# Performance work log

Measured on AMD Instinct MI355X. Metric: run time of the kernel, lower is better.

Reference implementation:

```python
import jax, jax.numpy as jnp
import numpy as np

B, T, D, H = 2, 2048, 1024, 16
HD = D // H

def setup_inputs() -> dict:
    key = jax.random.key(0)
    ks = jax.random.split(key, 5)
    fan = D
    bound_w = float(np.sqrt(6.0 / fan))  # kaiming_uniform-ish scale
    return {
        "x": jax.random.normal(ks[0], (B, T, D), dtype=jnp.float32),
        "W_qkv": jax.random.uniform(ks[1], (3 * D, D), minval=-bound_w, maxval=bound_w, dtype=jnp.float32),
        "b_qkv": jax.random.uniform(ks[2], (3 * D,), minval=-bound_w, maxval=bound_w, dtype=jnp.float32),
        "W_proj": jax.random.uniform(ks[3], (D, D), minval=-bound_w, maxval=bound_w, dtype=jnp.float32),
        "b_proj": jax.random.uniform(ks[4], (D,), minval=-bound_w, maxval=bound_w, dtype=jnp.float32),
    }

def reference(x, W_qkv, b_qkv, W_proj, b_proj):
    Bx, Tx, C = x.shape
    h, hd = H, C // H
    qkv = x @ W_qkv.T + b_qkv                      # (B,T,3C)
    q, k, v = jnp.split(qkv, 3, axis=-1)
    # (B,T,C) -> (B,h,T,hd)
    q = q.reshape(Bx, Tx, h, hd).transpose(0, 2, 1, 3)
    k = k.reshape(Bx, Tx, h, hd).transpose(0, 2, 1, 3)
    v = v.reshape(Bx, Tx, h, hd).transpose(0, 2, 1, 3)
    scale = hd ** -0.5
    scores = jnp.einsum('bhqd,bhkd->bhqk', q, k) * scale
    causal = jnp.tril(jnp.ones((Tx, Tx), dtype=bool))
    scores = jnp.where(causal, scores, -jnp.inf)
    weights = jax.nn.softmax(scores, axis=-1)      # stable softmax, same math
    out = jnp.einsum('bhqk,bhkd->bhqd', weights, v)
    out = out.transpose(0, 2, 1, 3).reshape(Bx, Tx, C)
    return out @ W_proj.T + b_proj
```

## Files before the change

kernel.cpp:

```cpp
#include <hip/hip_runtime.h>

typedef unsigned short u16;
typedef __attribute__((ext_vector_type(8))) short bf16x8;
typedef __attribute__((ext_vector_type(4))) short bf16x4;
typedef __attribute__((ext_vector_type(4))) float f32x4;

#define Bb 2
#define Tt 2048
#define Dd 1024
#define Hh 16
#define HD 64
#define NTOK (Bb*Tt)
#define QKVN (3*Dd)

__device__ __forceinline__ u16 f2b(float f) {
    unsigned u = __float_as_uint(f);
    unsigned r = (u + 0x7fffu + ((u >> 16) & 1u)) >> 16;
    return (u16)r;
}

__device__ __forceinline__ void g2l16(const u16* g, u16* l) {
    __builtin_amdgcn_global_load_lds(
        (const __attribute__((address_space(1))) unsigned int*)g,
        (__attribute__((address_space(3))) unsigned int*)l,
        16, 0, 0);
}

__device__ __forceinline__ unsigned pk2(float lo, float hi) {
    return __builtin_amdgcn_perm(__float_as_uint(hi), __float_as_uint(lo), 0x07060302u);
}

#define N4X  (NTOK * Dd / 4)
#define N4WQ (3 * Dd * Dd / 4)
#define N4WP (Dd * Dd / 4)
__global__ void cvt_all(const float* __restrict__ x, const float* __restrict__ wq,
                        const float* __restrict__ wp, u16* __restrict__ xb,
                        u16* __restrict__ wqb, u16* __restrict__ wpb) {
    int i = blockIdx.x * blockDim.x + threadIdx.x;
    const float* src; u16* dst; int j;
    if (i < N4X)                { src = x;  dst = xb;  j = i; }
    else if (i < N4X + N4WQ)    { src = wq; dst = wqb; j = i - N4X; }
    else                        { src = wp; dst = wpb; j = i - N4X - N4WQ; }
    float4 f = ((const float4*)src)[j];
    ushort4 o;
    o.x = f2b(f.x); o.y = f2b(f.y); o.z = f2b(f.z); o.w = f2b(f.w);
    ((ushort4*)dst)[j] = o;
}

#define TRS 136

__global__ __launch_bounds__(256, 3)
void gemm_qkv(const u16* __restrict__ A, const u16* __restrict__ Bt,
              const float* __restrict__ bias,
              u16* __restrict__ C16, u16* __restrict__ Vt) {
    const int N = QKVN, K = Dd;
    __shared__ alignas(16) u16 smem[128 * TRS];
    u16* As = smem;
    u16* Bs = smem + 8192;
    const int tid = threadIdx.x;
    const int wave = tid >> 6, lane = tid & 63;
    const int quad = lane >> 4, l16 = lane & 15;
    const int wm = (wave & 1) * 64, wn = (wave >> 1) * 64;
    const int m0 = blockIdx.x * 128, n0 = blockIdx.y * 128;
    const int lrow = lane >> 2, lcol = (lane & 3) << 3;

    f32x4 acc[4][4];
#pragma unroll
    for (int i = 0; i < 4; ++i)
#pragma unroll
        for (int j = 0; j < 4; ++j)
            acc[i][j] = (f32x4){0.f, 0.f, 0.f, 0.f};

    for (int k0 = 0; k0 < K; k0 += 64) {
#pragma unroll
        for (int h = 0; h < 2; ++h)
#pragma unroll
            for (int c = 0; c < 2; ++c) {
                const int rb = (c * 4 + wave) * 16;
                g2l16(A  + (size_t)(m0 + rb + lrow) * K + k0 + h * 32 + lcol,
                      &As[h * 4096 + rb * 32 + (lane << 3)]);
                g2l16(Bt + (size_t)(n0 + rb + lrow) * K + k0 + h * 32 + lcol,
                      &Bs[h * 4096 + rb * 32 + (lane << 3)]);
            }
        __syncthreads();
        bf16x8 a[4][2], b[4][2];
#pragma unroll
        for (int h = 0; h < 2; ++h) {
#pragma unroll
            for (int i = 0; i < 4; ++i)
                a[i][h] = *(const bf16x8*)(&As[h * 4096 + (wm + i * 16 + l16) * 32 + quad * 8]);
#pragma unroll
            for (int i = 0; i < 4; ++i)
                b[i][h] = *(const bf16x8*)(&Bs[h * 4096 + (wn + i * 16 + l16) * 32 + quad * 8]);
        }
#pragma unroll
        for (int h = 0; h < 2; ++h)
#pragma unroll
            for (int i = 0; i < 4; ++i)
#pragma unroll
                for (int j = 0; j < 4; ++j)
                    acc[i][j] = __builtin_amdgcn_mfma_f32_16x16x32_bf16(a[i][h], b[j][h], acc[i][j], 0, 0, 0);
        __syncthreads();
    }

    float b4[4];
#pragma unroll
    for (int j = 0; j < 4; ++j) b4[j] = bias[n0 + wn + j * 16 + l16];
    const bool isV = (n0 >= 2 * Dd);

    if (!isV) {
#pragma unroll
        for (int i = 0; i < 4; ++i)
#pragma unroll
            for (int j = 0; j < 4; ++j)
#pragma unroll
                for (int r = 0; r < 4; ++r) {
                    int m = m0 + wm + i * 16 + quad * 4 + r;
                    int n = n0 + wn + j * 16 + l16;
                    C16[(size_t)m * N + n] = f2b(acc[i][j][r] + b4[j]);
                }
    } else {
#pragma unroll
        for (int i = 0; i < 4; ++i)
#pragma unroll
            for (int j = 0; j < 4; ++j)
#pragma unroll
                for (int r = 0; r < 4; ++r) {
                    int ml = wm + i * 16 + quad * 4 + r;
                    int nl = wn + j * 16 + l16;
                    smem[nl * TRS + ml] = f2b(acc[i][j][r] + b4[j]);
                }
        __syncthreads();
        const int bidx = m0 >> 11, t0 = m0 & 2047;
        const int nl = tid >> 1, toff = (tid & 1) * 64;
        u16* dst = Vt + (size_t)bidx * (Hh * HD * Tt)
                      + (size_t)(n0 - 2 * Dd + nl) * Tt + t0 + toff;
        const u16* srcl = &smem[nl * TRS + toff];
#pragma unroll
        for (int k = 0; k < 8; ++k)
            *(uint4*)(dst + k * 8) = *(const uint4*)(srcl + k * 8);
    }
}

__global__ __launch_bounds__(256, 2)
void gemm_proj(const u16* __restrict__ A, const u16* __restrict__ Bt,
               const float* __restrict__ bias, float* __restrict__ Co) {
    const int N = Dd, K = Dd;
    __shared__ alignas(16) u16 As[2 * 128 * 32];
    __shared__ alignas(16) u16 Bs[2 * 64 * 32];
    const int tid = threadIdx.x;
    const int wave = tid >> 6, lane = tid & 63;
    const int quad = lane >> 4, l16 = lane & 15;
    const int wm = (wave & 1) * 64, wn = (wave >> 1) * 32;
    const int m0 = blockIdx.x * 128, n0 = blockIdx.y * 64;
    const int lrow = lane >> 2, lcol = (lane & 3) << 3;

    f32x4 acc[4][2];
#pragma unroll
    for (int i = 0; i < 4; ++i)
#pragma unroll
        for (int j = 0; j < 2; ++j)
            acc[i][j] = (f32x4){0.f, 0.f, 0.f, 0.f};

    for (int k0 = 0; k0 < K; k0 += 64) {
#pragma unroll
        for (int h = 0; h < 2; ++h) {
#pragma unroll
            for (int c = 0; c < 2; ++c) {
                const int rb = (c * 4 + wave) * 16;
                g2l16(A + (size_t)(m0 + rb + lrow) * K + k0 + h * 32 + lcol,
                      &As[h * 4096 + rb * 32 + (lane << 3)]);
            }
            g2l16(Bt + (size_t)(n0 + wave * 16 + lrow) * K + k0 + h * 32 + lcol,
                  &Bs[h * 2048 + (wave * 16) * 32 + (lane << 3)]);
        }
        __syncthreads();
        bf16x8 a[4][2], b[2][2];
#pragma unroll
        for (int h = 0; h < 2; ++h) {
#pragma unroll
            for (int i = 0; i < 4; ++i)
                a[i][h] = *(const bf16x8*)(&As[h * 4096 + (wm + i * 16 + l16) * 32 + quad * 8]);
#pragma unroll
            for (int j = 0; j < 2; ++j)
                b[j][h] = *(const bf16x8*)(&Bs[h * 2048 + (wn + j * 16 + l16) * 32 + quad * 8]);
        }
#pragma unroll
        for (int h = 0; h < 2; ++h)
#pragma unroll
            for (int i = 0; i < 4; ++i)
#pragma unroll
                for (int j = 0; j < 2; ++j)
                    acc[i][j] = __builtin_amdgcn_mfma_f32_16x16x32_bf16(a[i][h], b[j][h], acc[i][j], 0, 0, 0);
        __syncthreads();
    }

    float b2[2];
#pragma unroll
    for (int j = 0; j < 2; ++j) b2[j] = bias[n0 + wn + j * 16 + l16];

#pragma unroll
    for (int i = 0; i < 4; ++i)
#pragma unroll
        for (int j = 0; j < 2; ++j)
#pragma unroll
            for (int r = 0; r < 4; ++r) {
                int m = m0 + wm + i * 16 + quad * 4 + r;
                int n = n0 + wn + j * 16 + l16;
                Co[(size_t)m * N + n] = acc[i][j][r] + b2[j];
            }
}

#define LKP 80
#define FMX 24.0f

__global__ __launch_bounds__(256, 4)
void attn_fwd(const u16* __restrict__ qkv, const u16* __restrict__ Vt,
              u16* __restrict__ Ao) {
    const int bid = blockIdx.x;
    const int xcd = bid & 7, li = bid >> 3;
    const int bsub = li >> 5;
    const int vz = li & 31;
    const int zz = (vz & 1) ? (vz >> 1) : (31 - (vz >> 1));
    const int qt = (bsub & 1) ? (31 - zz) : zz;
    const int bh = (xcd << 2) | bsub;
    const int hh = bh & (Hh - 1), bidx = bh >> 4;
    const u16* Qp = qkv + (size_t)bidx * Tt * QKVN + hh * HD;
    const u16* Kp = Qp + Dd;
    const u16* Vp = Vt + (size_t)bh * HD * Tt;
    const int tid = threadIdx.x;
    const int wave = tid >> 6, lane = tid & 63;
    const int quad = lane >> 4, l16 = lane & 15;

    __shared__ alignas(16) u16 Ks[2][64 * LKP];
    __shared__ alignas(16) u16 Vs[2][64 * LKP];

    const int srow = tid >> 3, scol = (tid & 7) << 3;
    const int st0 = srow * LKP + scol, st1 = (srow + 32) * LKP + scol;
    const float sc = 0.125f * 1.44269504f;

    float mb[16];
#pragma unroll
    for (int nt = 0; nt < 4; ++nt)
#pragma unroll
        for (int r = 0; r < 4; ++r)
            mb[nt * 4 + r] = (nt * 16 + quad * 4 + r <= wave * 16 + l16) ? -FMX : -250.0f;

    const int qrow_g = qt * 64 + wave * 16 + l16;
    bf16x8 aq[2];
#pragma unroll
    for (int kk = 0; kk < 2; ++kk)
        aq[kk] = *(const bf16x8*)(Qp + (size_t)qrow_g * QKVN + kk * 32 + quad * 8);

    f32x4 o[4];
#pragma unroll
    for (int nt = 0; nt < 4; ++nt) o[nt] = (f32x4){0.f, 0.f, 0.f, 0.f};
    float lsum = 0.f;

    {
        uint4 k0r = *(const uint4*)(Kp + (size_t)srow * QKVN + scol);
        uint4 k1r = *(const uint4*)(Kp + (size_t)(srow + 32) * QKVN + scol);
        uint4 v0r = *(const uint4*)(Vp + (size_t)srow * Tt + scol);
        uint4 v1r = *(const uint4*)(Vp + (size_t)(srow + 32) * Tt + scol);
        *(uint4*)(&Ks[0][st0]) = k0r;
        *(uint4*)(&Ks[0][st1]) = k1r;
        *(uint4*)(&Vs[0][st0]) = v0r;
        *(uint4*)(&Vs[0][st1]) = v1r;
    }
    __syncthreads();

    const u16* kp0 = Kp + (size_t)(64 + srow) * QKVN + scol;
    const u16* kp1 = kp0 + (size_t)32 * QKVN;
    const u16* vp0 = Vp + (size_t)srow * Tt + 64 + scol;
    const u16* vp1 = vp0 + (size_t)32 * Tt;

    u16* Kcur = &Ks[0][0]; u16* Knxt = &Ks[1][0];
    u16* Vcur = &Vs[0][0]; u16* Vnxt = &Vs[1][0];

    for (int kt = 0; kt < qt; ++kt) {
        uint4 k0r = *(const uint4*)kp0;
        uint4 k1r = *(const uint4*)kp1;
        uint4 v0r = *(const uint4*)vp0;
        uint4 v1r = *(const uint4*)vp1;
        kp0 += (size_t)64 * QKVN; kp1 += (size_t)64 * QKVN;
        vp0 += 64; vp1 += 64;

        f32x4 s[4];
#pragma unroll
        for (int nt = 0; nt < 4; ++nt) {
            f32x4 z = (f32x4){0.f, 0.f, 0.f, 0.f};
#pragma unroll
            for (int kk = 0; kk < 2; ++kk) {
                bf16x8 ak = *(const bf16x8*)(&Kcur[(nt * 16 + l16) * LKP + kk * 32 + quad * 8]);
                z = __builtin_amdgcn_mfma_f32_16x16x32_bf16(ak, aq[kk], z, 0, 0, 0);
            }
            s[nt] = z;
        }

#pragma unroll
        for (int nt = 0; nt < 4; ++nt)
#pragma unroll
            for (int r = 0; r < 4; ++r) {
                float p = exp2f(__builtin_fmaf(s[nt][r], sc, -FMX));
                s[nt][r] = p;
                lsum += p;
            }

        bf16x4 ps[4];
#pragma unroll
        for (int nt = 0; nt < 4; ++nt) {
            uint2 w;
            w.x = pk2(s[nt][0], s[nt][1]);
            w.y = pk2(s[nt][2], s[nt][3]);
            ps[nt] = *(bf16x4*)&w;
        }

#pragma unroll
        for (int nt = 0; nt < 4; ++nt)
#pragma unroll
            for (int ntO = 0; ntO < 4; ++ntO) {
                bf16x4 av = *(const bf16x4*)(&Vcur[(ntO * 16 + l16) * LKP + nt * 16 + quad * 4]);
                o[ntO] = __builtin_amdgcn_mfma_f32_16x16x16bf16_1k(av, ps[nt], o[ntO], 0, 0, 0);
            }

        *(uint4*)(&Knxt[st0]) = k0r;
        *(uint4*)(&Knxt[st1]) = k1r;
        *(uint4*)(&Vnxt[st0]) = v0r;
        *(uint4*)(&Vnxt[st1]) = v1r;
        u16* t;
        t = Kcur; Kcur = Knxt; Knxt = t;
        t = Vcur; Vcur = Vnxt; Vnxt = t;
        __syncthreads();
    }

    {
        f32x4 s[4];
#pragma unroll
        for (int nt = 0; nt < 4; ++nt) {
            f32x4 z = (f32x4){0.f, 0.f, 0.f, 0.f};
#pragma unroll
            for (int kk = 0; kk < 2; ++kk) {
                bf16x8 ak = *(const bf16x8*)(&Kcur[(nt * 16 + l16) * LKP + kk * 32 + quad * 8]);
                z = __builtin_amdgcn_mfma_f32_16x16x32_bf16(ak, aq[kk], z, 0, 0, 0);
            }
            s[nt] = z;
        }
#pragma unroll
        for (int nt = 0; nt < 4; ++nt)
#pragma unroll
            for (int r = 0; r < 4; ++r) {
                float p = exp2f(__builtin_fmaf(s[nt][r], sc, mb[nt * 4 + r]));
                s[nt][r] = p;
                lsum += p;
            }
        bf16x4 ps[4];
#pragma unroll
        for (int nt = 0; nt < 4; ++nt) {
            uint2 w;
            w.x = pk2(s[nt][0], s[nt][1]);
            w.y = pk2(s[nt][2], s[nt][3]);
            ps[nt] = *(bf16x4*)&w;
        }
#pragma unroll
        for (int nt = 0; nt < 4; ++nt)
#pragma unroll
            for (int ntO = 0; ntO < 4; ++ntO) {
                bf16x4 av = *(const bf16x4*)(&Vcur[(ntO * 16 + l16) * LKP + nt * 16 + quad * 4]);
                o[ntO] = __builtin_amdgcn_mfma_f32_16x16x16bf16_1k(av, ps[nt], o[ntO], 0, 0, 0);
            }
    }

    lsum += __shfl_xor(lsum, 16, 64);
    lsum += __shfl_xor(lsum, 32, 64);
    const float rinv = 1.0f / lsum;
    u16* orow = Ao + ((size_t)bidx * Tt + qrow_g) * Dd + hh * HD;
#pragma unroll
    for (int nt = 0; nt < 4; ++nt) {
        ushort4 p4;
        p4.x = f2b(o[nt][0] * rinv); p4.y = f2b(o[nt][1] * rinv);
        p4.z = f2b(o[nt][2] * rinv); p4.w = f2b(o[nt][3] * rinv);
        *(ushort4*)(orow + nt * 16 + quad * 4) = p4;
    }
}

extern "C" void kernel_launch(void* const* d_in, const int* in_sizes, int n_in,
                              void* d_out, int out_size, void* d_ws, size_t ws_size,
                              hipStream_t stream) {
    const float* x      = (const float*)d_in[0];
    const float* W_qkv  = (const float*)d_in[1];
    const float* b_qkv  = (const float*)d_in[2];
    const float* W_proj = (const float*)d_in[3];
    const float* b_proj = (const float*)d_in[4];
    float* out = (float*)d_out;

    char* ws = (char*)d_ws;
    u16* Wprojb = (u16*)(ws);
    u16* Wqkvb  = (u16*)(ws + (2u << 20));
    u16* xb     = (u16*)(ws + (8u << 20));
    u16* qkvb   = (u16*)(ws + (16u << 20));
    u16* Vtb    = (u16*)(ws + (40u << 20));
    u16* attnb  = (u16*)(ws + (2u << 20));

    cvt_all<<<(N4X + N4WQ + N4WP) / 256, 256, 0, stream>>>(x, W_qkv, W_proj, xb, Wqkvb, Wprojb);

    {
        dim3 grid(NTOK / 128, QKVN / 128);
        gemm_qkv<<<grid, 256, 0, stream>>>(xb, Wqkvb, b_qkv, qkvb, Vtb);
    }
    {
        attn_fwd<<<dim3(1024), 256, 0, stream>>>(qkvb, Vtb, attnb);
    }
    {
        dim3 grid(NTOK / 128, Dd / 64);
        gemm_proj<<<grid, 256, 0, stream>>>(attnb, Wprojb, b_proj, out);
    }
}
```

Baseline: 180.1 us.

## Pair causal query tiles per block and XOR-swizzle V shared memory

```diff
diff --git a/kernel.cpp b/kernel.cpp
--- a/kernel.cpp
+++ b/kernel.cpp
@@ -214,16 +214,13 @@
 #define LKP 80
 #define FMX 24.0f
 
-__global__ __launch_bounds__(256, 4)
+__global__ __launch_bounds__(256, 3)
 void attn_fwd(const u16* __restrict__ qkv, const u16* __restrict__ Vt,
               u16* __restrict__ Ao) {
     const int bid = blockIdx.x;
     const int xcd = bid & 7, li = bid >> 3;
-    const int bsub = li >> 5;
-    const int vz = li & 31;
-    const int zz = (vz & 1) ? (vz >> 1) : (31 - (vz >> 1));
-    const int qt = (bsub & 1) ? (31 - zz) : zz;
-    const int bh = (xcd << 2) | bsub;
+    const int bh = (xcd << 2) | (li >> 4);
+    const int pair = li & 15;
     const int hh = bh & (Hh - 1), bidx = bh >> 4;
     const u16* Qp = qkv + (size_t)bidx * Tt * QKVN + hh * HD;
     const u16* Kp = Qp + Dd;
@@ -237,7 +234,16 @@
 
     const int srow = tid >> 3, scol = (tid & 7) << 3;
     const int st0 = srow * LKP + scol, st1 = (srow + 32) * LKP + scol;
+    const int svw = ((srow >> 2) & 3) << 3;
+    const int sv0 = srow * LKP + (scol ^ svw);
+    const int sv1 = (srow + 32) * LKP + (scol ^ svw);
     const float sc = 0.125f * 1.44269504f;
+
+    const int vswz = ((l16 >> 2) & 3) << 3;
+    int vcoff[4];
+#pragma unroll
+    for (int nt = 0; nt < 4; ++nt)
+        vcoff[nt] = (nt * 16 + quad * 4) ^ vswz;
 
     float mb[16];
 #pragma unroll
@@ -246,140 +252,144 @@
         for (int r = 0; r < 4; ++r)
             mb[nt * 4 + r] = (nt * 16 + quad * 4 + r <= wave * 16 + l16) ? -FMX : -250.0f;
 
-    const int qrow_g = qt * 64 + wave * 16 + l16;
-    bf16x8 aq[2];
-#pragma unroll
-    for (int kk = 0; kk < 2; ++kk)
-        aq[kk] = *(const bf16x8*)(Qp + (size_t)qrow_g * QKVN + kk * 32 + quad * 8);
-
-    f32x4 o[4];
-#pragma unroll
-    for (int nt = 0; nt < 4; ++nt) o[nt] = (f32x4){0.f, 0.f, 0.f, 0.f};
-    float lsum = 0.f;
-
-    {
-        uint4 k0r = *(const uint4*)(Kp + (size_t)srow * QKVN + scol);
-        uint4 k1r = *(const uint4*)(Kp + (size_t)(srow + 32) * QKVN + scol);
-        uint4 v0r = *(const uint4*)(Vp + (size_t)srow * Tt + scol);
-        uint4 v1r = *(const uint4*)(Vp + (size_t)(srow + 32) * Tt + scol);
-        *(uint4*)(&Ks[0][st0]) = k0r;
-        *(uint4*)(&Ks[0][st1]) = k1r;
-        *(uint4*)(&Vs[0][st0]) = v0r;
-        *(uint4*)(&Vs[0][st1]) = v1r;
-    }
-    __syncthreads();
-
-    const u16* kp0 = Kp + (size_t)(64 + srow) * QKVN + scol;
-    const u16* kp1 = kp0 + (size_t)32 * QKVN;
-    const u16* vp0 = Vp + (size_t)srow * Tt + 64 + scol;
-    const u16* vp1 = vp0 + (size_t)32 * Tt;
-
-    u16* Kcur = &Ks[0][0]; u16* Knxt = &Ks[1][0];
-    u16* Vcur = &Vs[0][0]; u16* Vnxt = &Vs[1][0];
-
-    for (int kt = 0; kt < qt; ++kt) {
-        uint4 k0r = *(const uint4*)kp0;
-        uint4 k1r = *(const uint4*)kp1;
-        uint4 v0r = *(const uint4*)vp0;
-        uint4 v1r = *(const uint4*)vp1;
-        kp0 += (size_t)64 * QKVN; kp1 += (size_t)64 * QKVN;
-        vp0 += 64; vp1 += 64;
-
-        f32x4 s[4];
+    for (int half = 0; half < 2; ++half) {
+        const int qt = half ? pair : (31 - pair);
+        const int qrow_g = qt * 64 + wave * 16 + l16;
+        bf16x8 aq[2];
+#pragma unroll
+        for (int kk = 0; kk < 2; ++kk)
+            aq[kk] = *(const bf16x8*)(Qp + (size_t)qrow_g * QKVN + kk * 32 + quad * 8);
+
+        f32x4 o[4];
+#pragma unroll
+        for (int nt = 0; nt < 4; ++nt) o[nt] = (f32x4){0.f, 0.f, 0.f, 0.f};
+        float lsum = 0.f;
+
+        {
+            uint4 k0r = *(const uint4*)(Kp + (size_t)srow * QKVN + scol);
+            uint4 k1r = *(const uint4*)(Kp + (size_t)(srow + 32) * QKVN + scol);
+            uint4 v0r = *(const uint4*)(Vp + (size_t)srow * Tt + scol);
+            uint4 v1r = *(const uint4*)(Vp + (size_t)(srow + 32) * Tt + scol);
+            *(uint4*)(&Ks[0][st0]) = k0r;
+            *(uint4*)(&Ks[0][st1]) = k1r;
+            *(uint4*)(&Vs[0][sv0]) = v0r;
+            *(uint4*)(&Vs[0][sv1]) = v1r;
+        }
+        __syncthreads();
+
+        const u16* kp0 = Kp + (size_t)(64 + srow) * QKVN + scol;
+        const u16* kp1 = kp0 + (size_t)32 * QKVN;
+        const u16* vp0 = Vp + (size_t)srow * Tt + 64 + scol;
+        const u16* vp1 = vp0 + (size_t)32 * Tt;
+
+        u16* Kcur = &Ks[0][0]; u16* Knxt = &Ks[1][0];
+        u16* Vcur = &Vs[0][0]; u16* Vnxt = &Vs[1][0];
+
+        for (int kt = 0; kt < qt; ++kt) {
+            uint4 k0r = *(const uint4*)kp0;
+            uint4 k1r = *(const uint4*)kp1;
+            uint4 v0r = *(const uint4*)vp0;
+            uint4 v1r = *(const uint4*)vp1;
+            kp0 += (size_t)64 * QKVN; kp1 += (size_t)64 * QKVN;
+            vp0 += 64; vp1 += 64;
+
+            f32x4 s[4];
+#pragma unroll
+            for (int nt = 0; nt < 4; ++nt) {
+                f32x4 z = (f32x4){0.f, 0.f, 0.f, 0.f};
+#pragma unroll
+                for (int kk = 0; kk < 2; ++kk) {
+                    bf16x8 ak = *(const bf16x8*)(&Kcur[(nt * 16 + l16) * LKP + kk * 32 + quad * 8]);
+                    z = __builtin_amdgcn_mfma_f32_16x16x32_bf16(ak, aq[kk], z, 0, 0, 0);
+                }
+                s[nt] = z;
+            }
+
+#pragma unroll
+            for (int nt = 0; nt < 4; ++nt)
+#pragma unroll
+                for (int r = 0; r < 4; ++r) {
+                    float p = exp2f(__builtin_fmaf(s[nt][r], sc, -FMX));
+                    s[nt][r] = p;
+                    lsum += p;
+                }
+
+            bf16x4 ps[4];
+#pragma unroll
+            for (int nt = 0; nt < 4; ++nt) {
+                uint2 w;
+                w.x = pk2(s[nt][0], s[nt][1]);
+                w.y = pk2(s[nt][2], s[nt][3]);
+                ps[nt] = *(bf16x4*)&w;
+            }
+
+#pragma unroll
+            for (int nt = 0; nt < 4; ++nt)
+#pragma unroll
+                for (int ntO = 0; ntO < 4; ++ntO) {
+                    bf16x4 av = *(const bf16x4*)(&Vcur[(ntO * 16 + l16) * LKP + vcoff[nt]]);
+                    o[ntO] = __builtin_amdgcn_mfma_f32_16x16x16bf16_1k(av, ps[nt], o[ntO], 0, 0, 0);
+                }
+
+            *(uint4*)(&Knxt[st0]) = k0r;
+            *(uint4*)(&Knxt[st1]) = k1r;
+            *(uint4*)(&Vnxt[sv0]) = v0r;
+            *(uint4*)(&Vnxt[sv1]) = v1r;
+            u16* t;
+            t = Kcur; Kcur = Knxt; Knxt = t;
+            t = Vcur; Vcur = Vnxt; Vnxt = t;
+            __syncthreads();
+        }
+
+        {
+            f32x4 s[4];
+#pragma unroll
+            for (int nt = 0; nt < 4; ++nt) {
+                f32x4 z = (f32x4){0.f, 0.f, 0.f, 0.f};
+#pragma unroll
+                for (int kk = 0; kk < 2; ++kk) {
+                    bf16x8 ak = *(const bf16x8*)(&Kcur[(nt * 16 + l16) * LKP + kk * 32 + quad * 8]);
+                    z = __builtin_amdgcn_mfma_f32_16x16x32_bf16(ak, aq[kk], z, 0, 0, 0);
+                }
+                s[nt] = z;
+            }
+#pragma unroll
+            for (int nt = 0; nt < 4; ++nt)
+#pragma unroll
+                for (int r = 0; r < 4; ++r) {
+                    float p = exp2f(__builtin_fmaf(s[nt][r], sc, mb[nt * 4 + r]));
+                    s[nt][r] = p;
+                    lsum += p;
+                }
+            bf16x4 ps[4];
+#pragma unroll
+            for (int nt = 0; nt < 4; ++nt) {
+                uint2 w;
+                w.x = pk2(s[nt][0], s[nt][1]);
+                w.y = pk2(s[nt][2], s[nt][3]);
+                ps[nt] = *(bf16x4*)&w;
+            }
+#pragma unroll
+            for (int nt = 0; nt < 4; ++nt)
+#pragma unroll
+                for (int ntO = 0; ntO < 4; ++ntO) {
+                    bf16x4 av = *(const bf16x4*)(&Vcur[(ntO * 16 + l16) * LKP + vcoff[nt]]);
+                    o[ntO] = __builtin_amdgcn_mfma_f32_16x16x16bf16_1k(av, ps[nt], o[ntO], 0, 0, 0);
+                }
+        }
+        __syncthreads();
+
+        lsum += __shfl_xor(lsum, 16, 64);
+        lsum += __shfl_xor(lsum, 32, 64);
+        const float rinv = 1.0f / lsum;
+        u16* orow = Ao + ((size_t)bidx * Tt + qrow_g) * Dd + hh * HD;
 #pragma unroll
         for (int nt = 0; nt < 4; ++nt) {
-            f32x4 z = (f32x4){0.f, 0.f, 0.f, 0.f};
-#pragma unroll
-            for (int kk = 0; kk < 2; ++kk) {
-                bf16x8 ak = *(const bf16x8*)(&Kcur[(nt * 16 + l16) * LKP + kk * 32 + quad * 8]);
-                z = __builtin_amdgcn_mfma_f32_16x16x32_bf16(ak, aq[kk], z, 0, 0, 0);
-            }
-            s[nt] = z;
-        }
-
-#pragma unroll
-        for (int nt = 0; nt < 4; ++nt)
-#pragma unroll
-            for (int r = 0; r < 4; ++r) {
-                float p = exp2f(__builtin_fmaf(s[nt][r], sc, -FMX));
-                s[nt][r] = p;
-                lsum += p;
-            }
-
-        bf16x4 ps[4];
-#pragma unroll
-        for (int nt = 0; nt < 4; ++nt) {
-            uint2 w;
-            w.x = pk2(s[nt][0], s[nt][1]);
-            w.y = pk2(s[nt][2], s[nt][3]);
-            ps[nt] = *(bf16x4*)&w;
-        }
-
-#pragma unroll
-        for (int nt = 0; nt < 4; ++nt)
-#pragma unroll
-            for (int ntO = 0; ntO < 4; ++ntO) {
-                bf16x4 av = *(const bf16x4*)(&Vcur[(ntO * 16 + l16) * LKP + nt * 16 + quad * 4]);
-                o[ntO] = __builtin_amdgcn_mfma_f32_16x16x16bf16_1k(av, ps[nt], o[ntO], 0, 0, 0);
-            }
-
-        *(uint4*)(&Knxt[st0]) = k0r;
-        *(uint4*)(&Knxt[st1]) = k1r;
-        *(uint4*)(&Vnxt[st0]) = v0r;
-        *(uint4*)(&Vnxt[st1]) = v1r;
-        u16* t;
-        t = Kcur; Kcur = Knxt; Knxt = t;
-        t = Vcur; Vcur = Vnxt; Vnxt = t;
-        __syncthreads();
-    }
-
-    {
-        f32x4 s[4];
-#pragma unroll
-        for (int nt = 0; nt < 4; ++nt) {
-            f32x4 z = (f32x4){0.f, 0.f, 0.f, 0.f};
-#pragma unroll
-            for (int kk = 0; kk < 2; ++kk) {
-                bf16x8 ak = *(const bf16x8*)(&Kcur[(nt * 16 + l16) * LKP + kk * 32 + quad * 8]);
-                z = __builtin_amdgcn_mfma_f32_16x16x32_bf16(ak, aq[kk], z, 0, 0, 0);
-            }
-            s[nt] = z;
-        }
-#pragma unroll
-        for (int nt = 0; nt < 4; ++nt)
-#pragma unroll
-            for (int r = 0; r < 4; ++r) {
-                float p = exp2f(__builtin_fmaf(s[nt][r], sc, mb[nt * 4 + r]));
-                s[nt][r] = p;
-                lsum += p;
-            }
-        bf16x4 ps[4];
-#pragma unroll
-        for (int nt = 0; nt < 4; ++nt) {
-            uint2 w;
-            w.x = pk2(s[nt][0], s[nt][1]);
-            w.y = pk2(s[nt][2], s[nt][3]);
-            ps[nt] = *(bf16x4*)&w;
-        }
-#pragma unroll
-        for (int nt = 0; nt < 4; ++nt)
-#pragma unroll
-            for (int ntO = 0; ntO < 4; ++ntO) {
-                bf16x4 av = *(const bf16x4*)(&Vcur[(ntO * 16 + l16) * LKP + nt * 16 + quad * 4]);
-                o[ntO] = __builtin_amdgcn_mfma_f32_16x16x16bf16_1k(av, ps[nt], o[ntO], 0, 0, 0);
-            }
-    }
-
-    lsum += __shfl_xor(lsum, 16, 64);
-    lsum += __shfl_xor(lsum, 32, 64);
-    const float rinv = 1.0f / lsum;
-    u16* orow = Ao + ((size_t)bidx * Tt + qrow_g) * Dd + hh * HD;
-#pragma unroll
-    for (int nt = 0; nt < 4; ++nt) {
-        ushort4 p4;
-        p4.x = f2b(o[nt][0] * rinv); p4.y = f2b(o[nt][1] * rinv);
-        p4.z = f2b(o[nt][2] * rinv); p4.w = f2b(o[nt][3] * rinv);
-        *(ushort4*)(orow + nt * 16 + quad * 4) = p4;
+            ushort4 p4;
+            p4.x = f2b(o[nt][0] * rinv); p4.y = f2b(o[nt][1] * rinv);
+            p4.z = f2b(o[nt][2] * rinv); p4.w = f2b(o[nt][3] * rinv);
+            *(ushort4*)(orow + nt * 16 + quad * 4) = p4;
+        }
     }
 }
 
@@ -408,7 +418,7 @@
         gemm_qkv<<<grid, 256, 0, stream>>>(xb, Wqkvb, b_qkv, qkvb, Vtb);
     }
     {
-        attn_fwd<<<dim3(1024), 256, 0, stream>>>(qkvb, Vtb, attnb);
+        attn_fwd<<<dim3(512), 256, 0, stream>>>(qkvb, Vtb, attnb);
     }
     {
         dim3 grid(NTOK / 128, Dd / 64);
```

Measured after the change: 174.9 us. 2.9% less time.
